# Kernel optimization log

Hardware: AMD Instinct MI355X
Metric: run time of the kernel (lower is better)

Reference implementation:

```python
import jax, jax.numpy as jnp
import numpy as np

B, S, D, H = 4, 1024, 1024, 16
HD = D // H  # head_dim = 64
NEG = -1e9  # stands in for float('-inf') in masked_fill; numerically safe


def setup_inputs() -> dict:
    key = jax.random.key(0)
    ks = jax.random.split(key, 8)
    q = jax.random.normal(ks[0], (B, S, D), dtype=jnp.float32)
    k = jax.random.normal(ks[1], (B, S, D), dtype=jnp.float32)
    v = jax.random.normal(ks[2], (B, S, D), dtype=jnp.float32)
    # padding mask: True marks padded positions; pad out the tail of each sequence
    pos = jnp.arange(S)
    lengths = jnp.array([S, S - 64, S - 128, S - 256])
    padding_mask = pos[None, :] >= lengths[:, None]  # [B, S] bool
    # additive causal mask: 0 on/below diagonal, NEG above
    causal_mask = jnp.where(jnp.tril(jnp.ones((S, S), dtype=bool)), 0.0, NEG).astype(jnp.float32)
    scale = 1.0 / np.sqrt(D)
    Wq = jax.random.normal(ks[3], (D, D), dtype=jnp.float32) * scale
    Wk = jax.random.normal(ks[4], (D, D), dtype=jnp.float32) * scale
    Wv = jax.random.normal(ks[5], (D, D), dtype=jnp.float32) * scale
    Wo = jax.random.normal(ks[6], (D, D), dtype=jnp.float32) * scale
    return {"q": q, "k": k, "v": v, "padding_mask": padding_mask,
            "causal_mask": causal_mask, "Wq": Wq, "Wk": Wk, "Wv": Wv,
            "Wo": Wo, "n_heads": H}


def reference(q, k, v, padding_mask, causal_mask, Wq, Wk, Wv, Wo, n_heads):
    b, s, d = q.shape
    hd = d // n_heads
    # projections (nn.Linear: x @ W^T, no bias)
    qp = (q @ Wq.T).reshape(b, s, n_heads, hd).transpose(0, 2, 1, 3)  # [b,h,s,hd]
    kp = (k @ Wk.T).reshape(b, s, n_heads, hd).transpose(0, 2, 1, 3)
    vp = (v @ Wv.T).reshape(b, s, n_heads, hd).transpose(0, 2, 1, 3)
    scores = jnp.einsum('bhqd,bhkd->bhqk', qp, kp) / jnp.sqrt(jnp.float32(hd))
    # masked_fill(padding_mask, -inf): mask broadcast over heads and query dim
    scores = jnp.where(padding_mask[:, None, None, :], NEG, scores)
    scores = scores + causal_mask  # additive causal mask
    attn = jax.nn.softmax(scores, axis=-1)
    out = jnp.einsum('bhqk,bhkd->bhqd', attn, vp)
    out = out.transpose(0, 2, 1, 3).reshape(b, s, d)
    return out @ Wo.T
```

## Files before the change

### kernel.cpp

```cpp
#include <hip/hip_runtime.h>
#include <hip/hip_bf16.h>

#define BB 4
#define SS 1024
#define DD 1024
#define HH 16
#define HD 64
#define MM (BB*SS)


typedef __bf16 bf16x8 __attribute__((ext_vector_type(8)));
typedef __bf16 bf16x4 __attribute__((ext_vector_type(4)));
typedef float  f32x4  __attribute__((ext_vector_type(4)));

__global__ __launch_bounds__(256) void expand_mask(const void* __restrict__ pmraw,
                                                   float* __restrict__ madd,
                                                   int n)
{
    const unsigned char* bytes = (const unsigned char*)pmraw;
    __shared__ int isbool;
    if (threadIdx.x == 0) isbool = 0;
    __syncthreads();
    int flag = 0;
    for (int idx = threadIdx.x; idx < n; idx += 256) {
        if ((idx & 3) && bytes[idx]) flag = 1;
    }
    if (flag) atomicOr(&isbool, 1);
    __syncthreads();
    int i = blockIdx.x * 256 + threadIdx.x;
    if (i < n) {
        int v = isbool ? (int)bytes[i] : ((const int*)pmraw)[i];
        madd[i] = (v != 0) ? -1e9f : 0.0f;
    }
}

__global__ __launch_bounds__(256) void convall(const float* __restrict__ q,
                                               const float* __restrict__ k,
                                               const float* __restrict__ v,
                                               const float* __restrict__ Wq,
                                               const float* __restrict__ Wk,
                                               const float* __restrict__ Wv,
                                               const float* __restrict__ Wo,
                                               __bf16* __restrict__ qb,
                                               __bf16* __restrict__ kb,
                                               __bf16* __restrict__ vb,
                                               __bf16* __restrict__ Wqb,
                                               __bf16* __restrict__ Wkb,
                                               __bf16* __restrict__ Wvb,
                                               __bf16* __restrict__ Wob)
{
    const float* s; __bf16* d; int i;
    if (blockIdx.y < 3) {
        if (blockIdx.y == 0)      { s = q; d = qb; }
        else if (blockIdx.y == 1) { s = k; d = kb; }
        else                      { s = v; d = vb; }
        i = (blockIdx.x * 256 + threadIdx.x) * 4;
    } else {
        const int wsel = blockIdx.x >> 10;
        const int lx   = blockIdx.x & 1023;
        if (wsel == 0)      { s = Wq; d = Wqb; }
        else if (wsel == 1) { s = Wk; d = Wkb; }
        else if (wsel == 2) { s = Wv; d = Wvb; }
        else                { s = Wo; d = Wob; }
        i = (lx * 256 + threadIdx.x) * 4;
    }
    float4 x = *(const float4*)(s + i);
    bf16x4 o;
    o[0] = (__bf16)x.x; o[1] = (__bf16)x.y;
    o[2] = (__bf16)x.z; o[3] = (__bf16)x.w;
    *(bf16x4*)(d + i) = o;
}

#define GM 128
#define GN 128
#define GK 64

__global__ __launch_bounds__(256) void gemm_qkv(const __bf16* __restrict__ qb,
                                                const __bf16* __restrict__ kb,
                                                const __bf16* __restrict__ vb,
                                                const __bf16* __restrict__ Wqb,
                                                const __bf16* __restrict__ Wkb,
                                                const __bf16* __restrict__ Wvb,
                                                __bf16* __restrict__ Qp,
                                                __bf16* __restrict__ Kp,
                                                __bf16* __restrict__ VpT)
{
    __shared__ __align__(16) __bf16 As[GM][GK];
    __shared__ __align__(16) __bf16 Bs[GN][GK];

    const __bf16 *A, *W; __bf16* C;
    const int z = blockIdx.z;
    if (z == 0)      { A = qb; W = Wqb; C = Qp;  }
    else if (z == 1) { A = kb; W = Wkb; C = Kp;  }
    else             { A = vb; W = Wvb; C = VpT; }

    const int tid  = threadIdx.x;
    const int lane = tid & 63;
    const int w    = tid >> 6;
    const int l15  = lane & 15;
    const int quad = lane >> 4;
    const int wr   = w >> 1;
    const int wc   = w & 1;

    const int m0 = blockIdx.x * GM;
    const int n0 = blockIdx.y * GN;

    const int srow = tid >> 3;
    const int scol = (tid & 7) * 8;
    const int gcol = (((tid & 7) ^ (srow & 7)) * 8);

    const __bf16* gA = A + (size_t)(m0 + srow) * DD + gcol;
    const __bf16* gB = W + (size_t)(n0 + srow) * DD + gcol;

    f32x4 acc[4][4] = {};

    for (int k0 = 0; k0 < DD; k0 += GK) {
        __syncthreads();
        #pragma unroll
        for (int c = 0; c < 4; ++c)
            __builtin_amdgcn_global_load_lds(
                (const __attribute__((address_space(1))) void*)(gA + (size_t)c * 32 * DD + k0),
                (__attribute__((address_space(3))) void*)(&As[c * 32 + srow][scol]), 16, 0, 0);
        #pragma unroll
        for (int c = 0; c < 4; ++c)
            __builtin_amdgcn_global_load_lds(
                (const __attribute__((address_space(1))) void*)(gB + (size_t)c * 32 * DD + k0),
                (__attribute__((address_space(3))) void*)(&Bs[c * 32 + srow][scol]), 16, 0, 0);
        __syncthreads();

        #pragma unroll
        for (int ks = 0; ks < 2; ++ks) {
            const int cidx = ((ks * 4 + quad) ^ (l15 & 7)) * 8;
            bf16x8 af[4], bf[4];
            #pragma unroll
            for (int mt = 0; mt < 4; ++mt)
                af[mt] = *(const bf16x8*)&As[wr * 64 + mt * 16 + l15][cidx];
            #pragma unroll
            for (int nt = 0; nt < 4; ++nt)
                bf[nt] = *(const bf16x8*)&Bs[wc * 64 + nt * 16 + l15][cidx];
            #pragma unroll
            for (int mt = 0; mt < 4; ++mt)
                #pragma unroll
                for (int nt = 0; nt < 4; ++nt)
                    acc[mt][nt] = __builtin_amdgcn_mfma_f32_16x16x32_bf16(
                        af[mt], bf[nt], acc[mt][nt], 0, 0, 0);
        }
    }

    if (z == 0) {
        #pragma unroll
        for (int mt = 0; mt < 4; ++mt)
            #pragma unroll
            for (int nt = 0; nt < 4; ++nt)
                #pragma unroll
                for (int r = 0; r < 4; ++r)
                    acc[mt][nt][r] *= 0.125f;
    }

    if (z == 2) {
        #pragma unroll
        for (int mt = 0; mt < 4; ++mt)
            #pragma unroll
            for (int nt = 0; nt < 4; ++nt) {
                bf16x4 o;
                #pragma unroll
                for (int r = 0; r < 4; ++r) o[r] = (__bf16)acc[mt][nt][r];
                const int n = n0 + wc * 64 + nt * 16 + l15;
                const int m = m0 + wr * 64 + mt * 16 + quad * 4;
                *(bf16x4*)&C[(size_t)n * MM + m] = o;
            }
    } else {
        #pragma unroll
        for (int mt = 0; mt < 4; ++mt)
            #pragma unroll
            for (int nt = 0; nt < 4; ++nt)
                #pragma unroll
                for (int r = 0; r < 4; ++r)
                    C[(size_t)(m0 + wr * 64 + mt * 16 + quad * 4 + r) * DD +
                      (n0 + wc * 64 + nt * 16 + l15)] = (__bf16)acc[mt][nt][r];
    }
}

__global__ __launch_bounds__(256) void gemm_wo(const __bf16* __restrict__ A,
                                               const __bf16* __restrict__ W,
                                               float* __restrict__ C)
{
    __shared__ __align__(16) __bf16 As[GM][GK];
    __shared__ __align__(16) __bf16 Bs[GN][GK];

    const int tid  = threadIdx.x;
    const int lane = tid & 63;
    const int w    = tid >> 6;
    const int l15  = lane & 15;
    const int quad = lane >> 4;
    const int wr   = w >> 1;
    const int wc   = w & 1;

    const int m0 = blockIdx.x * GM;
    const int n0 = blockIdx.y * GN;

    const int srow = tid >> 3;
    const int scol = (tid & 7) * 8;
    const int gcol = (((tid & 7) ^ (srow & 7)) * 8);

    const __bf16* gA = A + (size_t)(m0 + srow) * DD + gcol;
    const __bf16* gB = W + (size_t)(n0 + srow) * DD + gcol;

    f32x4 acc[4][4] = {};

    for (int k0 = 0; k0 < DD; k0 += GK) {
        __syncthreads();
        #pragma unroll
        for (int c = 0; c < 4; ++c)
            __builtin_amdgcn_global_load_lds(
                (const __attribute__((address_space(1))) void*)(gA + (size_t)c * 32 * DD + k0),
                (__attribute__((address_space(3))) void*)(&As[c * 32 + srow][scol]), 16, 0, 0);
        #pragma unroll
        for (int c = 0; c < 4; ++c)
            __builtin_amdgcn_global_load_lds(
                (const __attribute__((address_space(1))) void*)(gB + (size_t)c * 32 * DD + k0),
                (__attribute__((address_space(3))) void*)(&Bs[c * 32 + srow][scol]), 16, 0, 0);
        __syncthreads();

        #pragma unroll
        for (int ks = 0; ks < 2; ++ks) {
            const int cidx = ((ks * 4 + quad) ^ (l15 & 7)) * 8;
            bf16x8 af[4], bf[4];
            #pragma unroll
            for (int mt = 0; mt < 4; ++mt)
                af[mt] = *(const bf16x8*)&As[wr * 64 + mt * 16 + l15][cidx];
            #pragma unroll
            for (int nt = 0; nt < 4; ++nt)
                bf[nt] = *(const bf16x8*)&Bs[wc * 64 + nt * 16 + l15][cidx];
            #pragma unroll
            for (int mt = 0; mt < 4; ++mt)
                #pragma unroll
                for (int nt = 0; nt < 4; ++nt)
                    acc[mt][nt] = __builtin_amdgcn_mfma_f32_16x16x32_bf16(
                        af[mt], bf[nt], acc[mt][nt], 0, 0, 0);
        }
    }

    #pragma unroll
    for (int mt = 0; mt < 4; ++mt)
        #pragma unroll
        for (int nt = 0; nt < 4; ++nt)
            #pragma unroll
            for (int r = 0; r < 4; ++r)
                C[(size_t)(m0 + wr * 64 + mt * 16 + quad * 4 + r) * DD +
                  (n0 + wc * 64 + nt * 16 + l15)] = acc[mt][nt][r];
}

#define PSTR 72
#define OSTR 68

__global__ __launch_bounds__(256, 2) void flash_attn(const __bf16* __restrict__ Qp,
                                                     const __bf16* __restrict__ Kp,
                                                     const __bf16* __restrict__ VpT,
                                                     const float* __restrict__ maskadd,
                                                     __bf16* __restrict__ Op)
{
    __shared__ __align__(16) unsigned char smem[4 * 64 * PSTR * 2];
    __bf16 (*Pl)[64][PSTR]  = (__bf16 (*)[64][PSTR])smem;
    float  (*Obuf)[64][OSTR] = (float (*)[64][OSTR])smem;

    const int tid  = threadIdx.x;
    const int lane = tid & 63;
    const int w    = tid >> 6;
    const int l15  = lane & 15;
    const int quad = lane >> 4;
    const int h    = w & 1;
    const int tile = w >> 1;

    const int bh = blockIdx.x;
    const int hh = bh & (HH - 1);
    const int b  = bh >> 4;
    const int p  = blockIdx.y;
    const int m  = tile ? (15 - p) : p;

    const size_t hbase = (size_t)b * SS * DD + (size_t)hh * HD;
    const int q0 = m * 64;

    bf16x8 qf[4][2];
    #pragma unroll
    for (int qt = 0; qt < 4; ++qt) {
        const __bf16* qp = Qp + hbase + (size_t)(q0 + qt * 16 + l15) * DD + quad * 8;
        qf[qt][0] = *(const bf16x8*)qp;
        qf[qt][1] = *(const bf16x8*)(qp + 32);
    }

    const __bf16* vt = VpT + (size_t)(hh * HD) * MM + b * SS;
    const float* madd = maskadd + b * SS;

    f32x4 Ov[4][4] = {};
    float lsumq[4] = {};

    for (int kt = h; kt <= m; kt += 2) {
        const int kbase = kt * 64;
        const bool diag = (kt == m);

        f32x4 St[4][4];
        #pragma unroll
        for (int kg = 0; kg < 4; ++kg) {
            const __bf16* kp = Kp + hbase + (size_t)(kbase + kg * 16 + l15) * DD + quad * 8;
            bf16x8 kf0 = *(const bf16x8*)kp;
            bf16x8 kf1 = *(const bf16x8*)(kp + 32);
            #pragma unroll
            for (int qt = 0; qt < 4; ++qt) {
                f32x4 s = {};
                s = __builtin_amdgcn_mfma_f32_16x16x32_bf16(kf0, qf[qt][0], s, 0, 0, 0);
                s = __builtin_amdgcn_mfma_f32_16x16x32_bf16(kf1, qf[qt][1], s, 0, 0, 0);
                St[kg][qt] = s;
            }
        }

        bf16x8 vf[4][2];
        #pragma unroll
        for (int dt = 0; dt < 4; ++dt) {
            const __bf16* vp = vt + (size_t)(dt * 16 + l15) * MM + kbase + quad * 8;
            vf[dt][0] = *(const bf16x8*)vp;
            vf[dt][1] = *(const bf16x8*)(vp + 32);
        }

        #pragma unroll
        for (int kg = 0; kg < 4; ++kg) {
            const float4 mr = *(const float4*)&madd[kbase + kg * 16 + quad * 4];
            #pragma unroll
            for (int qt = 0; qt < 4; ++qt) {
                const int i = q0 + qt * 16 + l15;
                bf16x4 pk;
                #pragma unroll
                for (int r = 0; r < 4; ++r) {
                    const int j = kbase + kg * 16 + quad * 4 + r;
                    float pv = __expf(St[kg][qt][r] + ((const float*)&mr)[r]);
                    if (diag && j > i) pv = 0.f;
                    lsumq[qt] += pv;
                    pk[r] = (__bf16)pv;
                }
                *(bf16x4*)&Pl[w][qt * 16 + l15][kg * 16 + quad * 4] = pk;
            }
        }

        bf16x8 pf[4][2];
        #pragma unroll
        for (int qt = 0; qt < 4; ++qt) {
            pf[qt][0] = *(const bf16x8*)&Pl[w][qt * 16 + l15][quad * 8];
            pf[qt][1] = *(const bf16x8*)&Pl[w][qt * 16 + l15][quad * 8 + 32];
        }

        #pragma unroll
        for (int dt = 0; dt < 4; ++dt) {
            #pragma unroll
            for (int qt = 0; qt < 4; ++qt) {
                Ov[qt][dt] = __builtin_amdgcn_mfma_f32_16x16x32_bf16(pf[qt][0], vf[dt][0], Ov[qt][dt], 0, 0, 0);
                Ov[qt][dt] = __builtin_amdgcn_mfma_f32_16x16x32_bf16(pf[qt][1], vf[dt][1], Ov[qt][dt], 0, 0, 0);
            }
        }
    }

    #pragma unroll
    for (int off = 16; off < 64; off <<= 1)
        #pragma unroll
        for (int qt = 0; qt < 4; ++qt)
            lsumq[qt] += __shfl_xor(lsumq[qt], off);

    __syncthreads();
    if (h == 1) {
        #pragma unroll
        for (int qt = 0; qt < 4; ++qt) {
            #pragma unroll
            for (int dt = 0; dt < 4; ++dt)
                #pragma unroll
                for (int r = 0; r < 4; ++r)
                    Obuf[tile][qt * 16 + quad * 4 + r][dt * 16 + l15] = Ov[qt][dt][r];
            if (quad == 0)
                Obuf[tile][qt * 16 + l15][64] = lsumq[qt];
        }
    }
    __syncthreads();
    if (h == 0) {
        #pragma unroll
        for (int qt = 0; qt < 4; ++qt) {
            const float rcp = 1.0f / (lsumq[qt] + Obuf[tile][qt * 16 + l15][64]);
            float rq[4];
            #pragma unroll
            for (int r = 0; r < 4; ++r) rq[r] = __shfl(rcp, quad * 4 + r);
            #pragma unroll
            for (int dt = 0; dt < 4; ++dt)
                #pragma unroll
                for (int r = 0; r < 4; ++r) {
                    const int i = q0 + qt * 16 + quad * 4 + r;
                    float o = Ov[qt][dt][r] +
                              Obuf[tile][qt * 16 + quad * 4 + r][dt * 16 + l15];
                    Op[hbase + (size_t)i * DD + dt * 16 + l15] = (__bf16)(o * rq[r]);
                }
        }
    }
}

extern "C" void kernel_launch(void* const* d_in, const int* in_sizes, int n_in,
                              void* d_out, int out_size, void* d_ws, size_t ws_size,
                              hipStream_t stream)
{
    const float* q  = (const float*)d_in[0];
    const float* k  = (const float*)d_in[1];
    const float* v  = (const float*)d_in[2];
    const void*  pm = d_in[3];
    const float* Wq = (const float*)d_in[5];
    const float* Wk = (const float*)d_in[6];
    const float* Wv = (const float*)d_in[7];
    const float* Wo = (const float*)d_in[8];

    char* ws = (char*)d_ws;
    float* madd = (float*)ws;
    const size_t MB = 1024 * 1024;
    char* base = ws + 65536;

    __bf16* qb  = (__bf16*)(base +  0 * MB);
    __bf16* kb  = (__bf16*)(base +  8 * MB);
    __bf16* vb  = (__bf16*)(base + 16 * MB);
    __bf16* Wqb = (__bf16*)(base + 24 * MB);
    __bf16* Wkb = (__bf16*)(base + 26 * MB);
    __bf16* Wvb = (__bf16*)(base + 28 * MB);
    __bf16* Wob = (__bf16*)(base + 30 * MB);
    __bf16* Qp  = (__bf16*)(base + 32 * MB);
    __bf16* Kp  = (__bf16*)(base + 40 * MB);
    __bf16* VpT = (__bf16*)(base + 48 * MB);
    __bf16* Op  = qb;

    float* out = (float*)d_out;
    const int NT = MM * DD;

    expand_mask<<<(BB * SS) / 256, 256, 0, stream>>>(pm, madd, BB * SS);
    convall<<<dim3(NT / 1024, 4), 256, 0, stream>>>(q, k, v, Wq, Wk, Wv, Wo,
                                                    qb, kb, vb, Wqb, Wkb, Wvb, Wob);

    dim3 gg(MM / GM, DD / GN, 3);
    gemm_qkv<<<gg, 256, 0, stream>>>(qb, kb, vb, Wqb, Wkb, Wvb, Qp, Kp, VpT);

    dim3 ga(BB * HH, 8);
    flash_attn<<<ga, 256, 0, stream>>>(Qp, Kp, VpT, madd, Op);

    dim3 gw(MM / GM, DD / GN);
    gemm_wo<<<gw, 256, 0, stream>>>(Op, Wob, out);
}
```

Baseline: 221.2 us.

## Load GEMM B fragments directly from global memory and defer V loads in attention

```diff
diff --git a/kernel.cpp b/kernel.cpp
--- a/kernel.cpp
+++ b/kernel.cpp
@@ -86,7 +86,6 @@
                                                 __bf16* __restrict__ VpT)
 {
     __shared__ __align__(16) __bf16 As[GM][GK];
-    __shared__ __align__(16) __bf16 Bs[GN][GK];
 
     const __bf16 *A, *W; __bf16* C;
     const int z = blockIdx.z;
@@ -110,7 +109,7 @@
     const int gcol = (((tid & 7) ^ (srow & 7)) * 8);
 
     const __bf16* gA = A + (size_t)(m0 + srow) * DD + gcol;
-    const __bf16* gB = W + (size_t)(n0 + srow) * DD + gcol;
+    const __bf16* gB = W + (size_t)(n0 + wc * 64 + l15) * DD + quad * 8;
 
     f32x4 acc[4][4] = {};
 
@@ -121,29 +120,28 @@
             __builtin_amdgcn_global_load_lds(
                 (const __attribute__((address_space(1))) void*)(gA + (size_t)c * 32 * DD + k0),
                 (__attribute__((address_space(3))) void*)(&As[c * 32 + srow][scol]), 16, 0, 0);
-        #pragma unroll
-        for (int c = 0; c < 4; ++c)
-            __builtin_amdgcn_global_load_lds(
-                (const __attribute__((address_space(1))) void*)(gB + (size_t)c * 32 * DD + k0),
-                (__attribute__((address_space(3))) void*)(&Bs[c * 32 + srow][scol]), 16, 0, 0);
         __syncthreads();
+
+        bf16x8 bfr[2][4];
+        #pragma unroll
+        for (int ks = 0; ks < 2; ++ks)
+            #pragma unroll
+            for (int nt = 0; nt < 4; ++nt)
+                bfr[ks][nt] = *(const bf16x8*)(gB + (size_t)nt * 16 * DD + k0 + ks * 32);
 
         #pragma unroll
         for (int ks = 0; ks < 2; ++ks) {
             const int cidx = ((ks * 4 + quad) ^ (l15 & 7)) * 8;
-            bf16x8 af[4], bf[4];
+            bf16x8 af[4];
             #pragma unroll
             for (int mt = 0; mt < 4; ++mt)
                 af[mt] = *(const bf16x8*)&As[wr * 64 + mt * 16 + l15][cidx];
             #pragma unroll
-            for (int nt = 0; nt < 4; ++nt)
-                bf[nt] = *(const bf16x8*)&Bs[wc * 64 + nt * 16 + l15][cidx];
-            #pragma unroll
             for (int mt = 0; mt < 4; ++mt)
                 #pragma unroll
                 for (int nt = 0; nt < 4; ++nt)
                     acc[mt][nt] = __builtin_amdgcn_mfma_f32_16x16x32_bf16(
-                        af[mt], bf[nt], acc[mt][nt], 0, 0, 0);
+                        af[mt], bfr[ks][nt], acc[mt][nt], 0, 0, 0);
         }
     }
 
@@ -181,12 +179,11 @@
     }
 }
 
-__global__ __launch_bounds__(256) void gemm_wo(const __bf16* __restrict__ A,
+__global__ __launch_bounds__(256) void gemm_wo(const __bf16* __restrict__ Ain,
                                                const __bf16* __restrict__ W,
                                                float* __restrict__ C)
 {
     __shared__ __align__(16) __bf16 As[GM][GK];
-    __shared__ __align__(16) __bf16 Bs[GN][GK];
 
     const int tid  = threadIdx.x;
     const int lane = tid & 63;
@@ -203,8 +200,8 @@
     const int scol = (tid & 7) * 8;
     const int gcol = (((tid & 7) ^ (srow & 7)) * 8);
 
-    const __bf16* gA = A + (size_t)(m0 + srow) * DD + gcol;
-    const __bf16* gB = W + (size_t)(n0 + srow) * DD + gcol;
+    const __bf16* gA = Ain + (size_t)(m0 + srow) * DD + gcol;
+    const __bf16* gB = W   + (size_t)(n0 + wc * 64 + l15) * DD + quad * 8;
 
     f32x4 acc[4][4] = {};
 
@@ -215,29 +212,28 @@
             __builtin_amdgcn_global_load_lds(
                 (const __attribute__((address_space(1))) void*)(gA + (size_t)c * 32 * DD + k0),
                 (__attribute__((address_space(3))) void*)(&As[c * 32 + srow][scol]), 16, 0, 0);
-        #pragma unroll
-        for (int c = 0; c < 4; ++c)
-            __builtin_amdgcn_global_load_lds(
-                (const __attribute__((address_space(1))) void*)(gB + (size_t)c * 32 * DD + k0),
-                (__attribute__((address_space(3))) void*)(&Bs[c * 32 + srow][scol]), 16, 0, 0);
         __syncthreads();
+
+        bf16x8 bfr[2][4];
+        #pragma unroll
+        for (int ks = 0; ks < 2; ++ks)
+            #pragma unroll
+            for (int nt = 0; nt < 4; ++nt)
+                bfr[ks][nt] = *(const bf16x8*)(gB + (size_t)nt * 16 * DD + k0 + ks * 32);
 
         #pragma unroll
         for (int ks = 0; ks < 2; ++ks) {
             const int cidx = ((ks * 4 + quad) ^ (l15 & 7)) * 8;
-            bf16x8 af[4], bf[4];
+            bf16x8 af[4];
             #pragma unroll
             for (int mt = 0; mt < 4; ++mt)
                 af[mt] = *(const bf16x8*)&As[wr * 64 + mt * 16 + l15][cidx];
             #pragma unroll
-            for (int nt = 0; nt < 4; ++nt)
-                bf[nt] = *(const bf16x8*)&Bs[wc * 64 + nt * 16 + l15][cidx];
-            #pragma unroll
             for (int mt = 0; mt < 4; ++mt)
                 #pragma unroll
                 for (int nt = 0; nt < 4; ++nt)
                     acc[mt][nt] = __builtin_amdgcn_mfma_f32_16x16x32_bf16(
-                        af[mt], bf[nt], acc[mt][nt], 0, 0, 0);
+                        af[mt], bfr[ks][nt], acc[mt][nt], 0, 0, 0);
         }
     }
 
@@ -312,14 +308,6 @@
                 s = __builtin_amdgcn_mfma_f32_16x16x32_bf16(kf1, qf[qt][1], s, 0, 0, 0);
                 St[kg][qt] = s;
             }
-        }
-
-        bf16x8 vf[4][2];
-        #pragma unroll
-        for (int dt = 0; dt < 4; ++dt) {
-            const __bf16* vp = vt + (size_t)(dt * 16 + l15) * MM + kbase + quad * 8;
-            vf[dt][0] = *(const bf16x8*)vp;
-            vf[dt][1] = *(const bf16x8*)(vp + 32);
         }
 
         #pragma unroll
@@ -350,10 +338,13 @@
 
         #pragma unroll
         for (int dt = 0; dt < 4; ++dt) {
+            const __bf16* vp = vt + (size_t)(dt * 16 + l15) * MM + kbase + quad * 8;
+            bf16x8 vf0 = *(const bf16x8*)vp;
+            bf16x8 vf1 = *(const bf16x8*)(vp + 32);
             #pragma unroll
             for (int qt = 0; qt < 4; ++qt) {
-                Ov[qt][dt] = __builtin_amdgcn_mfma_f32_16x16x32_bf16(pf[qt][0], vf[dt][0], Ov[qt][dt], 0, 0, 0);
-                Ov[qt][dt] = __builtin_amdgcn_mfma_f32_16x16x32_bf16(pf[qt][1], vf[dt][1], Ov[qt][dt], 0, 0, 0);
+                Ov[qt][dt] = __builtin_amdgcn_mfma_f32_16x16x32_bf16(pf[qt][0], vf0, Ov[qt][dt], 0, 0, 0);
+                Ov[qt][dt] = __builtin_amdgcn_mfma_f32_16x16x32_bf16(pf[qt][1], vf1, Ov[qt][dt], 0, 0, 0);
             }
         }
     }
```

New measurement: 260.8 us. +17.9%, slower.
